# Kernel tuning notes

Hardware: AMD Instinct MI355X
Metric: run time of the kernel (lower is better)

The kernel has to match this reference:

```python
import jax, jax.numpy as jnp
import numpy as np

N = 50000      # nodes
E = 800000     # random edges (self-loops added in reference, per PyG GATConv default)
F_IN = 128
B = 512        # graphs in the batch
NEG_SLOPE = 0.2  # PyG GATConv leaky_relu default


def setup_inputs() -> dict:
    key = jax.random.key(0)
    ks = jax.random.split(key, 12)
    def w(k, shape, fan_in):
        return jax.random.normal(k, shape, jnp.float32) / np.sqrt(fan_in)
    return {
        "x": jax.random.normal(ks[0], (N, F_IN), jnp.float32),
        "edge_index": jax.random.randint(ks[1], (2, E), 0, N, dtype=jnp.int32),
        "batch": jnp.sort(jax.random.randint(ks[2], (N,), 0, B, dtype=jnp.int32)),
        "W1": w(ks[3], (F_IN, 4 * 64), F_IN),
        "a_src1": w(ks[4], (4, 64), 64),
        "a_dst1": w(ks[5], (4, 64), 64),
        "b1": jnp.zeros((4 * 64,), jnp.float32),
        "W2": w(ks[6], (256, 1 * 128), 256),
        "a_src2": w(ks[7], (1, 128), 128),
        "a_dst2": w(ks[8], (1, 128), 128),
        "b2": jnp.zeros((128,), jnp.float32),
        "Wl": w(ks[9], (128, 1), 128),
        "bl": jnp.zeros((1,), jnp.float32),
    }


def gat_layer(x, src, dst, W, a_src, a_dst, b, n):
    H, Fo = a_src.shape
    h = (x @ W).reshape(n, H, Fo)                      # [N,H,Fo]
    alpha_s = jnp.einsum("nhf,hf->nh", h, a_src)       # [N,H]
    alpha_d = jnp.einsum("nhf,hf->nh", h, a_dst)
    e = jax.nn.leaky_relu(alpha_s[src] + alpha_d[dst], NEG_SLOPE)  # [E,H]
    # segment softmax over incoming edges of each dst node
    m = jax.ops.segment_max(e, dst, num_segments=n)    # [N,H]; self-loops => every node hit
    ex = jnp.exp(e - m[dst])
    den = jax.ops.segment_sum(ex, dst, num_segments=n)
    alpha = ex / den[dst]                              # [E,H]
    out = jax.ops.segment_sum(h[src] * alpha[:, :, None], dst, num_segments=n)
    return out.reshape(n, H * Fo) + b


def reference(x, edge_index, batch, W1, a_src1, a_dst1, b1, W2, a_src2, a_dst2, b2, Wl, bl):
    n = x.shape[0]
    loops = jnp.arange(n, dtype=edge_index.dtype)
    src = jnp.concatenate([edge_index[0], loops])
    dst = jnp.concatenate([edge_index[1], loops])
    h = jax.nn.elu(gat_layer(x, src, dst, W1, a_src1, a_dst1, b1, n))
    h = jax.nn.elu(gat_layer(h, src, dst, W2, a_src2, a_dst2, b2, n))
    # dropout omitted (inference)
    sums = jax.ops.segment_sum(h, batch, num_segments=B)
    cnt = jax.ops.segment_sum(jnp.ones((n,), h.dtype), batch, num_segments=B)
    g = sums / jnp.maximum(cnt, 1.0)[:, None]          # global_mean_pool -> [B,128]
    return jax.nn.sigmoid(g @ Wl + bl).reshape(-1)     # [B]
```

## Files before the change

kernel.cpp:

```cpp
#include <hip/hip_runtime.h>
#include <hip/hip_bf16.h>

#define NN 50000
#define EE 800000
#define ETOT 850000
#define BB 512
#define CAP 64
#define NPART 8
#define DPP 6250
#define SCAT_BLKS 2048

typedef __hip_bfloat16 bf16;
typedef __attribute__((ext_vector_type(8))) __bf16 v8bf;
typedef __attribute__((ext_vector_type(4))) float f32x4;

__device__ __forceinline__ float lo2f(unsigned int u) {
    return __uint_as_float(u << 16);
}
__device__ __forceinline__ float hi2f(unsigned int u) {
    return __uint_as_float(u & 0xffff0000u);
}
__device__ __forceinline__ float us2f(unsigned short u) {
    return __uint_as_float(((unsigned int)u) << 16);
}
__device__ __forceinline__ unsigned short f2bfbits(float f) {
    bf16 h = __float2bfloat16(f);
    return *reinterpret_cast<unsigned short*>(&h);
}
__device__ __forceinline__ float lrelu_exp(float ev) {
    ev = ev > 0.f ? ev : 0.2f * ev;
    return __expf(fminf(ev, 80.f));
}

__global__ void k_prep(const float* __restrict__ W1, const float* __restrict__ W2,
                       bf16* __restrict__ wt1, bf16* __restrict__ wt2,
                       int* __restrict__ deg) {
    int idx = blockIdx.x * blockDim.x + threadIdx.x;
    if (idx < 256 * 128) {
        int c = idx >> 7, k = idx & 127;
        wt1[idx] = __float2bfloat16(W1[k * 256 + c]);
    } else {
        int j = idx - 256 * 128;
        int c = j >> 8, k = j & 255;
        wt2[j] = __float2bfloat16(W2[k * 128 + c]);
    }
    if (idx < NN) deg[idx] = 0;
}

__global__ __launch_bounds__(256, 2)
void k_scatter_gemm1(const int* __restrict__ srcArr, const int* __restrict__ dstArr,
                     int* __restrict__ deg, unsigned short* __restrict__ csrc,
                     const float* __restrict__ x, const bf16* __restrict__ wt1,
                     const float* __restrict__ aw_s, const float* __restrict__ aw_d,
                     bf16* __restrict__ h1, float* __restrict__ as1,
                     float* __restrict__ ad1) {
    __shared__ bf16 xs[32 * 136];
    if (blockIdx.x < SCAT_BLKS) {
        int part = blockIdx.x & (NPART - 1);
        int lo = part * DPP;
        int t = threadIdx.x;
        const int STRIDE = (SCAT_BLKS >> 3) * 256;
        for (int e = (blockIdx.x >> 3) * 256 + t; e < ETOT; e += STRIDE) {
            int d, s;
            if (e < EE) { d = dstArr[e]; s = srcArr[e]; }
            else        { d = e - EE;    s = d; }
            d = min(max(d, 0), NN - 1);
            s = min(max(s, 0), NN - 1);
            if (d >= lo && d < lo + DPP) {
                int p = atomicAdd(&deg[d], 1);
                if (p < CAP) csrc[d * CAP + p] = (unsigned short)s;
            }
        }
        return;
    }

    int bid = blockIdx.x - SCAT_BLKS;
    int n0 = bid * 32;
    int t = threadIdx.x;
    for (int i = 0; i < 4; i++) {
        int idx = t + 256 * i;
        int r = idx >> 5, c4 = idx & 31;
        float4 v = make_float4(0.f, 0.f, 0.f, 0.f);
        if (n0 + r < NN) v = *(const float4*)(x + (size_t)(n0 + r) * 128 + c4 * 4);
        ushort4 o;
        o.x = f2bfbits(v.x); o.y = f2bfbits(v.y);
        o.z = f2bfbits(v.z); o.w = f2bfbits(v.w);
        *(ushort4*)(&xs[r * 136 + c4 * 4]) = o;
    }
    __syncthreads();

    int wv = t >> 6, lane = t & 63;
    int q = lane >> 4, r16 = lane & 15;
    int rowBase = (wv & 1) * 16;
    int colBase = (wv >> 1) * 128;

    f32x4 acc[8];
#pragma unroll
    for (int ct = 0; ct < 8; ct++) acc[ct] = (f32x4){0.f, 0.f, 0.f, 0.f};

#pragma unroll
    for (int kt = 0; kt < 4; kt++) {
        v8bf va = *(const v8bf*)(&xs[(rowBase + r16) * 136 + kt * 32 + q * 8]);
#pragma unroll
        for (int ct = 0; ct < 8; ct++) {
            v8bf vb = *(const v8bf*)(wt1 + (size_t)(colBase + ct * 16 + r16) * 128 + kt * 32 + q * 8);
            acc[ct] = __builtin_amdgcn_mfma_f32_16x16x32_bf16(va, vb, acc[ct], 0, 0, 0);
        }
    }

    float wsv[8], wdv[8];
#pragma unroll
    for (int ct = 0; ct < 8; ct++) {
        int col = colBase + ct * 16 + r16;
        wsv[ct] = aw_s[col];
        wdv[ct] = aw_d[col];
    }

    float ps[4][2], pd[4][2];
#pragma unroll
    for (int reg = 0; reg < 4; reg++) {
        ps[reg][0] = 0.f; ps[reg][1] = 0.f;
        pd[reg][0] = 0.f; pd[reg][1] = 0.f;
    }

#pragma unroll
    for (int reg = 0; reg < 4; reg++) {
        int node = n0 + rowBase + q * 4 + reg;
        bool ok = node < NN;
#pragma unroll
        for (int ct = 0; ct < 8; ct++) {
            float v = acc[ct][reg];
            if (ok) h1[(size_t)node * 256 + colBase + ct * 16 + r16] = __float2bfloat16(v);
            ps[reg][ct >> 2] += v * wsv[ct];
            pd[reg][ct >> 2] += v * wdv[ct];
        }
    }

#pragma unroll
    for (int reg = 0; reg < 4; reg++) {
        int node = n0 + rowBase + q * 4 + reg;
        bool ok = node < NN;
#pragma unroll
        for (int lh = 0; lh < 2; lh++) {
            float a = ps[reg][lh], b = pd[reg][lh];
            for (int mask = 1; mask <= 8; mask <<= 1) {
                a += __shfl_xor(a, mask);
                b += __shfl_xor(b, mask);
            }
            if (r16 == 0 && ok) {
                int head = (wv >> 1) * 2 + lh;
                as1[node * 4 + head] = a;
                ad1[node * 4 + head] = b;
            }
        }
    }
}

__global__ void k_gather1(const unsigned short* __restrict__ csrc, const int* __restrict__ deg,
                          const bf16* __restrict__ h1, const float* __restrict__ as1,
                          const float* __restrict__ ad1, const float* __restrict__ b1,
                          bf16* __restrict__ x2) {
    int bid = blockIdx.x;
    int n = bid >> 1, slice = bid & 1;
    int t = threadIdx.x;
    int lh = t >> 5;
    int cnt = min(deg[n], CAP);
    float2 ad = *(const float2*)&ad1[n * 4 + slice * 2];
    __shared__ unsigned int ls[CAP];
    __shared__ float la[CAP * 2];
    const char* h1c = (const char*)h1;
    unsigned int tconst = (unsigned int)(slice * 128 + t * 2) * 2;
    if (t < cnt) {
        int s = (int)csrc[n * CAP + t];
        ls[t] = (unsigned int)s << 9;
        float2 as = *(const float2*)&as1[s * 4 + slice * 2];
        la[t * 2 + 0] = lrelu_exp(as.x + ad.x);
        la[t * 2 + 1] = lrelu_exp(as.y + ad.y);
    }
    __syncthreads();
    float a0 = 0.f, a1 = 0.f, ssum = 0.f;
    int j = 0;
    for (; j + 3 < cnt; j += 4) {
        unsigned int o0 = ls[j] + tconst, o1 = ls[j + 1] + tconst;
        unsigned int o2 = ls[j + 2] + tconst, o3 = ls[j + 3] + tconst;
        float A0 = la[j * 2 + lh], A1 = la[j * 2 + 2 + lh];
        float A2 = la[j * 2 + 4 + lh], A3 = la[j * 2 + 6 + lh];
        unsigned int u0 = *(const unsigned int*)(h1c + o0);
        unsigned int u1 = *(const unsigned int*)(h1c + o1);
        unsigned int u2 = *(const unsigned int*)(h1c + o2);
        unsigned int u3 = *(const unsigned int*)(h1c + o3);
        ssum += (A0 + A1) + (A2 + A3);
        a0 = fmaf(A0, lo2f(u0), a0); a0 = fmaf(A1, lo2f(u1), a0);
        a0 = fmaf(A2, lo2f(u2), a0); a0 = fmaf(A3, lo2f(u3), a0);
        a1 = fmaf(A0, hi2f(u0), a1); a1 = fmaf(A1, hi2f(u1), a1);
        a1 = fmaf(A2, hi2f(u2), a1); a1 = fmaf(A3, hi2f(u3), a1);
    }
    for (; j < cnt; j++) {
        unsigned int o0 = ls[j] + tconst;
        float A0 = la[j * 2 + lh];
        unsigned int u0 = *(const unsigned int*)(h1c + o0);
        ssum += A0;
        a0 = fmaf(A0, lo2f(u0), a0);
        a1 = fmaf(A0, hi2f(u0), a1);
    }
    float inv = 1.f / fmaxf(ssum, 1e-35f);
    int c = slice * 128 + t * 2;
    float r0 = a0 * inv + b1[c + 0];
    float r1 = a1 * inv + b1[c + 1];
    r0 = r0 > 0.f ? r0 : (__expf(r0) - 1.f);
    r1 = r1 > 0.f ? r1 : (__expf(r1) - 1.f);
    unsigned int packed = (unsigned int)f2bfbits(r0) | ((unsigned int)f2bfbits(r1) << 16);
    *(unsigned int*)((unsigned short*)x2 + (size_t)n * 256 + c) = packed;
}

__global__ __launch_bounds__(256, 2)
void k_gemm2(const bf16* __restrict__ x2, const bf16* __restrict__ wt2,
             const float* __restrict__ aw_s, const float* __restrict__ aw_d,
             bf16* __restrict__ h2, float* __restrict__ as2,
             float* __restrict__ ad2) {
    int n0 = blockIdx.x * 32;
    int t = threadIdx.x;
    __shared__ bf16 xs[32 * 264];
    __shared__ float psPart[32][2];
    __shared__ float pdPart[32][2];
    for (int i = 0; i < 4; i++) {
        int idx = t + 256 * i;
        int r = idx >> 5, c8 = idx & 31;
        uint4 v;
        if (n0 + r < NN) v = *(const uint4*)(x2 + (size_t)(n0 + r) * 256 + c8 * 8);
        else             v = make_uint4(0, 0, 0, 0);
        *(uint4*)(&xs[r * 264 + c8 * 8]) = v;
    }
    __syncthreads();

    int wv = t >> 6, lane = t & 63;
    int q = lane >> 4, r16 = lane & 15;
    int rowBase = (wv & 1) * 16;
    int colBase = (wv >> 1) * 64;

    f32x4 acc[4];
#pragma unroll
    for (int ct = 0; ct < 4; ct++) acc[ct] = (f32x4){0.f, 0.f, 0.f, 0.f};

#pragma unroll
    for (int kt = 0; kt < 8; kt++) {
        v8bf va = *(const v8bf*)(&xs[(rowBase + r16) * 264 + kt * 32 + q * 8]);
#pragma unroll
        for (int ct = 0; ct < 4; ct++) {
            v8bf vb = *(const v8bf*)(wt2 + (size_t)(colBase + ct * 16 + r16) * 256 + kt * 32 + q * 8);
            acc[ct] = __builtin_amdgcn_mfma_f32_16x16x32_bf16(va, vb, acc[ct], 0, 0, 0);
        }
    }

    float wsv[4], wdv[4];
#pragma unroll
    for (int ct = 0; ct < 4; ct++) {
        int col = colBase + ct * 16 + r16;
        wsv[ct] = aw_s[col];
        wdv[ct] = aw_d[col];
    }

#pragma unroll
    for (int reg = 0; reg < 4; reg++) {
        int node = n0 + rowBase + q * 4 + reg;
        bool ok = node < NN;
        float ps = 0.f, pd = 0.f;
#pragma unroll
        for (int ct = 0; ct < 4; ct++) {
            float v = acc[ct][reg];
            if (ok) h2[(size_t)node * 128 + colBase + ct * 16 + r16] = __float2bfloat16(v);
            ps += v * wsv[ct];
            pd += v * wdv[ct];
        }
        for (int mask = 1; mask <= 8; mask <<= 1) {
            ps += __shfl_xor(ps, mask);
            pd += __shfl_xor(pd, mask);
        }
        if (r16 == 0) {
            int li = rowBase + q * 4 + reg;
            psPart[li][wv >> 1] = ps;
            pdPart[li][wv >> 1] = pd;
        }
    }
    __syncthreads();
    if (t < 32) {
        int node = n0 + t;
        if (node < NN) {
            as2[node] = psPart[t][0] + psPart[t][1];
            ad2[node] = pdPart[t][0] + pdPart[t][1];
        }
    }
}

__global__ void k_gather2(const unsigned short* __restrict__ csrc, const int* __restrict__ deg,
                          const bf16* __restrict__ h2, const float* __restrict__ as2,
                          const float* __restrict__ ad2, const float* __restrict__ b2,
                          bf16* __restrict__ hf) {
    int n = blockIdx.x;
    int t = threadIdx.x;
    int cnt = min(deg[n], CAP);
    float adn = ad2[n];
    __shared__ unsigned int ls[CAP];
    __shared__ float la[CAP];
    const char* h2c = (const char*)h2;
    unsigned int tconst = (unsigned int)t * 4;
    if (t < cnt) {
        int s = (int)csrc[n * CAP + t];
        ls[t] = (unsigned int)s << 8;
        la[t] = lrelu_exp(as2[s] + adn);
    }
    __syncthreads();
    float a0 = 0.f, a1 = 0.f, ssum = 0.f;
    int j = 0;
    for (; j + 3 < cnt; j += 4) {
        unsigned int o0 = ls[j] + tconst, o1 = ls[j + 1] + tconst;
        unsigned int o2 = ls[j + 2] + tconst, o3 = ls[j + 3] + tconst;
        float A0 = la[j], A1 = la[j + 1], A2 = la[j + 2], A3 = la[j + 3];
        unsigned int u0 = *(const unsigned int*)(h2c + o0);
        unsigned int u1 = *(const unsigned int*)(h2c + o1);
        unsigned int u2 = *(const unsigned int*)(h2c + o2);
        unsigned int u3 = *(const unsigned int*)(h2c + o3);
        ssum += (A0 + A1) + (A2 + A3);
        a0 = fmaf(A0, lo2f(u0), a0); a0 = fmaf(A1, lo2f(u1), a0);
        a0 = fmaf(A2, lo2f(u2), a0); a0 = fmaf(A3, lo2f(u3), a0);
        a1 = fmaf(A0, hi2f(u0), a1); a1 = fmaf(A1, hi2f(u1), a1);
        a1 = fmaf(A2, hi2f(u2), a1); a1 = fmaf(A3, hi2f(u3), a1);
    }
    for (; j < cnt; j++) {
        unsigned int o0 = ls[j] + tconst;
        float A0 = la[j];
        unsigned int u0 = *(const unsigned int*)(h2c + o0);
        ssum += A0;
        a0 = fmaf(A0, lo2f(u0), a0);
        a1 = fmaf(A0, hi2f(u0), a1);
    }
    float inv = 1.f / fmaxf(ssum, 1e-35f);
    int c = t * 2;
    float r0 = a0 * inv + b2[c + 0];
    float r1 = a1 * inv + b2[c + 1];
    r0 = r0 > 0.f ? r0 : (__expf(r0) - 1.f);
    r1 = r1 > 0.f ? r1 : (__expf(r1) - 1.f);
    unsigned int packed = (unsigned int)f2bfbits(r0) | ((unsigned int)f2bfbits(r1) << 16);
    *(unsigned int*)((unsigned short*)hf + (size_t)n * 128 + c) = packed;
}

__global__ void k_pool(const bf16* __restrict__ hf, const int* __restrict__ batch,
                       const float* __restrict__ Wl, const float* __restrict__ bl,
                       float* __restrict__ out) {
    int b = blockIdx.x;
    int t = threadIdx.x;
    int lo = 0, hi = NN;
    while (lo < hi) { int m = (lo + hi) >> 1; if (batch[m] < b) lo = m + 1; else hi = m; }
    int start = lo;
    int lo2 = start, hi2 = NN;
    while (lo2 < hi2) { int m = (lo2 + hi2) >> 1; if (batch[m] < b + 1) lo2 = m + 1; else hi2 = m; }
    int end = lo2;
    const unsigned short* hu = (const unsigned short*)hf;
    float sum = 0.f;
    for (int n = start; n < end; n++) sum += us2f(hu[(size_t)n * 128 + t]);
    int c = end - start;
    float g = sum / (float)(c > 0 ? c : 1);
    float p = g * Wl[t];
    for (int o = 32; o > 0; o >>= 1) p += __shfl_down(p, o);
    __shared__ float red[2];
    if ((t & 63) == 0) red[t >> 6] = p;
    __syncthreads();
    if (t == 0) {
        float acc = red[0] + red[1] + bl[0];
        out[b] = 1.f / (1.f + __expf(-acc));
    }
}

extern "C" void kernel_launch(void* const* d_in, const int* in_sizes, int n_in,
                              void* d_out, int out_size, void* d_ws, size_t ws_size,
                              hipStream_t stream) {
    const float* x = (const float*)d_in[0];
    const int* ei = (const int*)d_in[1];
    const int* batch = (const int*)d_in[2];
    const float* W1 = (const float*)d_in[3];
    const float* aw_s1 = (const float*)d_in[4];
    const float* aw_d1 = (const float*)d_in[5];
    const float* b1 = (const float*)d_in[6];
    const float* W2 = (const float*)d_in[7];
    const float* aw_s2 = (const float*)d_in[8];
    const float* aw_d2 = (const float*)d_in[9];
    const float* b2 = (const float*)d_in[10];
    const float* Wl = (const float*)d_in[11];
    const float* bl = (const float*)d_in[12];
    const int* srcArr = ei;
    const int* dstArr = ei + EE;

    char* w = (char*)d_ws;
    size_t off = 0;
    auto alloc = [&](size_t bytes) -> void* {
        void* p = (void*)(w + off);
        off = (off + bytes + 255) & ~(size_t)255;
        return p;
    };
    bf16* bufA = (bf16*)alloc((size_t)NN * 256 * 2);
    bf16* bufB = (bf16*)alloc((size_t)NN * 256 * 2);
    unsigned short* csrc = (unsigned short*)alloc((size_t)NN * CAP * 2);
    float* as1 = (float*)alloc((size_t)NN * 4 * 4);
    float* ad1 = (float*)alloc((size_t)NN * 4 * 4);
    float* as2 = (float*)alloc((size_t)NN * 4);
    float* ad2 = (float*)alloc((size_t)NN * 4);
    int* deg = (int*)alloc((size_t)NN * 4);
    bf16* wt1 = (bf16*)alloc((size_t)256 * 128 * 2);
    bf16* wt2 = (bf16*)alloc((size_t)128 * 256 * 2);
    (void)ws_size;

    k_prep<<<256, 256, 0, stream>>>(W1, W2, wt1, wt2, deg);

    bf16* h1 = bufA;
    bf16* x2 = bufB;
    int gemmBlocks = (NN + 31) / 32;
    k_scatter_gemm1<<<SCAT_BLKS + gemmBlocks, 256, 0, stream>>>(
        srcArr, dstArr, deg, csrc, x, wt1, aw_s1, aw_d1, h1, as1, ad1);

    k_gather1<<<NN * 2, 64, 0, stream>>>(csrc, deg, h1, as1, ad1, b1, x2);

    bf16* h2 = bufA;
    k_gemm2<<<gemmBlocks, 256, 0, stream>>>(x2, wt2, aw_s2, aw_d2, h2, as2, ad2);

    bf16* hf = bufB;
    k_gather2<<<NN, 64, 0, stream>>>(csrc, deg, h2, as2, ad2, b2, hf);

    k_pool<<<BB, 128, 0, stream>>>(hf, batch, Wl, bl, (float*)d_out);
}
```

Baseline: 329.4 us.

## Fuse layer-2 gather with mean-pool via atomics; simplify edge scatter partitioning

The layer-2 gather kernel now handles 8 nodes per 512-thread block and accumulates ELU outputs directly into per-graph sums with float atomics, replacing the separate pool kernel's serial per-graph loop over node rows and the bf16 hf write/read. A small output kernel divides the sums by the node counts and applies the linear layer and sigmoid. The edge scatter also drops its 8-way destination partitioning, which re-read every edge once per partition, in favour of one thread per edge doing a direct atomic insert. This adds atomic contention on deg, makes the pooled sums' summation order nondeterministic, and changes the order of CSR entries within each node.

Result: faster. 310.0 us (-5.9%).

```diff
diff --git a/kernel.cpp b/kernel.cpp
--- a/kernel.cpp
+++ b/kernel.cpp
@@ -6,9 +6,7 @@
 #define ETOT 850000
 #define BB 512
 #define CAP 64
-#define NPART 8
-#define DPP 6250
-#define SCAT_BLKS 2048
+#define SCAT_BLKS ((ETOT + 255) / 256)
 
 typedef __hip_bfloat16 bf16;
 typedef __attribute__((ext_vector_type(8))) __bf16 v8bf;
@@ -34,7 +32,7 @@
 
 __global__ void k_prep(const float* __restrict__ W1, const float* __restrict__ W2,
                        bf16* __restrict__ wt1, bf16* __restrict__ wt2,
-                       int* __restrict__ deg) {
+                       int* __restrict__ deg, float* __restrict__ gsum) {
     int idx = blockIdx.x * blockDim.x + threadIdx.x;
     if (idx < 256 * 128) {
         int c = idx >> 7, k = idx & 127;
@@ -45,6 +43,7 @@
         wt2[j] = __float2bfloat16(W2[k * 128 + c]);
     }
     if (idx < NN) deg[idx] = 0;
+    gsum[idx] = 0.f;
 }
 
 __global__ __launch_bounds__(256, 2)
@@ -56,20 +55,15 @@
                      float* __restrict__ ad1) {
     __shared__ bf16 xs[32 * 136];
     if (blockIdx.x < SCAT_BLKS) {
-        int part = blockIdx.x & (NPART - 1);
-        int lo = part * DPP;
-        int t = threadIdx.x;
-        const int STRIDE = (SCAT_BLKS >> 3) * 256;
-        for (int e = (blockIdx.x >> 3) * 256 + t; e < ETOT; e += STRIDE) {
+        int e = blockIdx.x * 256 + threadIdx.x;
+        if (e < ETOT) {
             int d, s;
             if (e < EE) { d = dstArr[e]; s = srcArr[e]; }
             else        { d = e - EE;    s = d; }
             d = min(max(d, 0), NN - 1);
             s = min(max(s, 0), NN - 1);
-            if (d >= lo && d < lo + DPP) {
-                int p = atomicAdd(&deg[d], 1);
-                if (p < CAP) csrc[d * CAP + p] = (unsigned short)s;
-            }
+            int p = atomicAdd(&deg[d], 1);
+            if (p < CAP) csrc[d * CAP + p] = (unsigned short)s;
         }
         return;
     }
@@ -292,30 +286,35 @@
     }
 }
 
-__global__ void k_gather2(const unsigned short* __restrict__ csrc, const int* __restrict__ deg,
-                          const bf16* __restrict__ h2, const float* __restrict__ as2,
-                          const float* __restrict__ ad2, const float* __restrict__ b2,
-                          bf16* __restrict__ hf) {
-    int n = blockIdx.x;
-    int t = threadIdx.x;
+__global__ __launch_bounds__(512, 2)
+void k_gather2pool(const unsigned short* __restrict__ csrc, const int* __restrict__ deg,
+                   const bf16* __restrict__ h2, const float* __restrict__ as2,
+                   const float* __restrict__ ad2, const float* __restrict__ b2,
+                   const int* __restrict__ batch, float* __restrict__ gsum) {
+    int wv = threadIdx.x >> 6;
+    int t = threadIdx.x & 63;
+    int n = blockIdx.x * 8 + wv;
     int cnt = min(deg[n], CAP);
     float adn = ad2[n];
-    __shared__ unsigned int ls[CAP];
-    __shared__ float la[CAP];
+    __shared__ unsigned int ls[8][CAP];
+    __shared__ float la[8][CAP];
+    __shared__ float acc[8][128];
     const char* h2c = (const char*)h2;
     unsigned int tconst = (unsigned int)t * 4;
     if (t < cnt) {
         int s = (int)csrc[n * CAP + t];
-        ls[t] = (unsigned int)s << 8;
-        la[t] = lrelu_exp(as2[s] + adn);
-    }
-    __syncthreads();
+        ls[wv][t] = (unsigned int)s << 8;
+        la[wv][t] = lrelu_exp(as2[s] + adn);
+    }
+    __syncthreads();
+    const unsigned int* lsw = ls[wv];
+    const float* law = la[wv];
     float a0 = 0.f, a1 = 0.f, ssum = 0.f;
     int j = 0;
     for (; j + 3 < cnt; j += 4) {
-        unsigned int o0 = ls[j] + tconst, o1 = ls[j + 1] + tconst;
-        unsigned int o2 = ls[j + 2] + tconst, o3 = ls[j + 3] + tconst;
-        float A0 = la[j], A1 = la[j + 1], A2 = la[j + 2], A3 = la[j + 3];
+        unsigned int o0 = lsw[j] + tconst, o1 = lsw[j + 1] + tconst;
+        unsigned int o2 = lsw[j + 2] + tconst, o3 = lsw[j + 3] + tconst;
+        float A0 = law[j], A1 = law[j + 1], A2 = law[j + 2], A3 = law[j + 3];
         unsigned int u0 = *(const unsigned int*)(h2c + o0);
         unsigned int u1 = *(const unsigned int*)(h2c + o1);
         unsigned int u2 = *(const unsigned int*)(h2c + o2);
@@ -327,8 +326,8 @@
         a1 = fmaf(A2, hi2f(u2), a1); a1 = fmaf(A3, hi2f(u3), a1);
     }
     for (; j < cnt; j++) {
-        unsigned int o0 = ls[j] + tconst;
-        float A0 = la[j];
+        unsigned int o0 = lsw[j] + tconst;
+        float A0 = law[j];
         unsigned int u0 = *(const unsigned int*)(h2c + o0);
         ssum += A0;
         a0 = fmaf(A0, lo2f(u0), a0);
@@ -340,13 +339,29 @@
     float r1 = a1 * inv + b2[c + 1];
     r0 = r0 > 0.f ? r0 : (__expf(r0) - 1.f);
     r1 = r1 > 0.f ? r1 : (__expf(r1) - 1.f);
-    unsigned int packed = (unsigned int)f2bfbits(r0) | ((unsigned int)f2bfbits(r1) << 16);
-    *(unsigned int*)((unsigned short*)hf + (size_t)n * 128 + c) = packed;
-}
-
-__global__ void k_pool(const bf16* __restrict__ hf, const int* __restrict__ batch,
-                       const float* __restrict__ Wl, const float* __restrict__ bl,
-                       float* __restrict__ out) {
+    acc[wv][c] = r0;
+    acc[wv][c + 1] = r1;
+    __syncthreads();
+    int tt = threadIdx.x;
+    if (tt < 128) {
+        int n0 = blockIdx.x * 8;
+        int b0 = batch[n0], b7 = batch[n0 + 7];
+        if (b0 == b7) {
+            float s = 0.f;
+#pragma unroll
+            for (int w = 0; w < 8; w++) s += acc[w][tt];
+            atomicAdd(&gsum[b0 * 128 + tt], s);
+        } else {
+#pragma unroll
+            for (int w = 0; w < 8; w++)
+                atomicAdd(&gsum[batch[n0 + w] * 128 + tt], acc[w][tt]);
+        }
+    }
+}
+
+__global__ void k_out(const float* __restrict__ gsum, const int* __restrict__ batch,
+                      const float* __restrict__ Wl, const float* __restrict__ bl,
+                      float* __restrict__ out) {
     int b = blockIdx.x;
     int t = threadIdx.x;
     int lo = 0, hi = NN;
@@ -354,12 +369,8 @@
     int start = lo;
     int lo2 = start, hi2 = NN;
     while (lo2 < hi2) { int m = (lo2 + hi2) >> 1; if (batch[m] < b + 1) lo2 = m + 1; else hi2 = m; }
-    int end = lo2;
-    const unsigned short* hu = (const unsigned short*)hf;
-    float sum = 0.f;
-    for (int n = start; n < end; n++) sum += us2f(hu[(size_t)n * 128 + t]);
-    int c = end - start;
-    float g = sum / (float)(c > 0 ? c : 1);
+    int cnt = lo2 - start;
+    float g = gsum[b * 128 + t] / (float)(cnt > 0 ? cnt : 1);
     float p = g * Wl[t];
     for (int o = 32; o > 0; o >>= 1) p += __shfl_down(p, o);
     __shared__ float red[2];
@@ -405,11 +416,12 @@
     float* as2 = (float*)alloc((size_t)NN * 4);
     float* ad2 = (float*)alloc((size_t)NN * 4);
     int* deg = (int*)alloc((size_t)NN * 4);
+    float* gsum = (float*)alloc((size_t)BB * 128 * 4);
     bf16* wt1 = (bf16*)alloc((size_t)256 * 128 * 2);
     bf16* wt2 = (bf16*)alloc((size_t)128 * 256 * 2);
     (void)ws_size;
 
-    k_prep<<<256, 256, 0, stream>>>(W1, W2, wt1, wt2, deg);
+    k_prep<<<256, 256, 0, stream>>>(W1, W2, wt1, wt2, deg, gsum);
 
     bf16* h1 = bufA;
     bf16* x2 = bufB;
@@ -422,8 +434,7 @@
     bf16* h2 = bufA;
     k_gemm2<<<gemmBlocks, 256, 0, stream>>>(x2, wt2, aw_s2, aw_d2, h2, as2, ad2);
 
-    bf16* hf = bufB;
-    k_gather2<<<NN, 64, 0, stream>>>(csrc, deg, h2, as2, ad2, b2, hf);
-
-    k_pool<<<BB, 128, 0, stream>>>(hf, batch, Wl, bl, (float*)d_out);
-}
+    k_gather2pool<<<NN / 8, 512, 0, stream>>>(csrc, deg, h2, as2, ad2, b2, batch, gsum);
+
+    k_out<<<BB, 128, 0, stream>>>(gsum, batch, Wl, bl, (float*)d_out);
+}
```
